# Optimization experiments

Measured on AMD Instinct MI355X. Metric: run time of the kernel, lower is better.

## Reference

```python
import jax, jax.numpy as jnp
import numpy as np

N = 50000      # nodes
E = 1600000    # edges (avg degree 32)
D_IN = 128
HID = 64


def setup_inputs() -> dict:
    key = jax.random.key(0)
    ks = jax.random.split(key, 7)
    x = jax.random.normal(ks[0], (N, D_IN), dtype=jnp.float32)
    ei = jax.random.randint(ks[1], (2, E), 0, N, dtype=jnp.int32)
    ew = jax.random.uniform(ks[2], (E,), dtype=jnp.float32)
    # GCNConv linear weights (glorot-ish scale); lin has no bias, conv bias added post-aggregation
    W1 = jax.random.normal(ks[3], (HID, D_IN), dtype=jnp.float32) * (1.0 / np.sqrt(D_IN))
    b1 = jnp.zeros((HID,), dtype=jnp.float32)
    W2 = jax.random.normal(ks[4], (HID, HID), dtype=jnp.float32) * (1.0 / np.sqrt(HID))
    b2 = jnp.zeros((HID,), dtype=jnp.float32)
    return {"x": x, "ei": ei, "ew": ew, "W1": W1, "b1": b1, "W2": W2, "b2": b2}


def _gcn_conv(x, src, dst, ew_all, W, b, n_nodes):
    """PyG GCNConv: gcn_norm (self-loops already appended) + x@W.T, gather-scale-scatter, +b."""
    deg = jax.ops.segment_sum(ew_all, dst, num_segments=n_nodes)  # dst-side weighted degree
    dinv = jnp.where(deg > 0, jax.lax.rsqrt(deg), 0.0)            # deg^{-1/2}, inf->0
    norm = dinv[src] * ew_all * dinv[dst]                          # [E+N]
    h = x @ W.T                                                    # [N, hid]
    msg = h[src] * norm[:, None]                                   # gather + scale
    out = jax.ops.segment_sum(msg, dst, num_segments=n_nodes)     # scatter-add
    return out + b


def reference(x, ei, ew, W1, b1, W2, b2):
    n_nodes = x.shape[0]
    # add self loops once (fill value 1.0), shared by both conv layers
    loop = jnp.arange(n_nodes, dtype=ei.dtype)
    src = jnp.concatenate([ei[0], loop])
    dst = jnp.concatenate([ei[1], loop])
    ew_all = jnp.concatenate([ew, jnp.ones((n_nodes,), dtype=ew.dtype)])

    h1 = jax.nn.relu(_gcn_conv(x, src, dst, ew_all, W1, b1, n_nodes))
    # dropout is identity in eval mode
    h2 = _gcn_conv(h1, src, dst, ew_all, W2, b2, n_nodes)
    return h2 + h1
```

## Files before the change

### kernel.cpp

```cpp
#include <hip/hip_runtime.h>

#define HID 64
#define DIN 128
#define NBLK 512

typedef unsigned long long ull;
typedef unsigned short u16;

static __device__ __forceinline__ u16 f2bf(float f) {
  unsigned u = __float_as_uint(f);
  unsigned lsb = (u >> 16) & 1u;
  u += 0x7fffu + lsb;
  return (u16)(u >> 16);
}


__global__ __launch_bounds__(512) void k_histA(const int* __restrict__ dst,
                                               int* __restrict__ G,
                                               int E, int NBC, int chunk,
                                               const float* __restrict__ W1,
                                               const float* __restrict__ W2,
                                               float* __restrict__ WT1,
                                               float* __restrict__ WT2) {
  int b = blockIdx.x, tid = threadIdx.x;
  if (b >= NBLK) {
    int idx = (b - NBLK) * 512 + tid;
    if (idx < DIN * 64) {
      int d = idx >> 6, j = idx & 63;
      WT1[idx] = W1[j * DIN + d];
    }
    int i2 = idx - DIN * 64;
    if (i2 >= 0 && i2 < HID * 64) {
      int d = i2 >> 6, j = i2 & 63;
      WT2[i2] = W2[j * HID + d];
    }
    return;
  }
  __shared__ int h[256];
  if (tid < 256) h[tid] = 0;
  __syncthreads();
  int e0 = b * chunk, e1 = min(E, e0 + chunk);
  for (int e = e0 + tid; e < e1; e += 512) atomicAdd(&h[dst[e] >> 8], 1);
  __syncthreads();
  if (tid < NBC) G[tid * NBLK + b] = h[tid];
}


__global__ __launch_bounds__(256) void k_chunksum(const int* __restrict__ G, int* bsum, int L) {
  int b = blockIdx.x, t = threadIdx.x;
  int base = b * 2048;
  int s = 0;
  for (int i = t; i < 2048; i += 256) {
    int g = base + i;
    s += (g < L) ? G[g] : 0;
  }
  __shared__ int red[4];
  for (int o = 32; o > 0; o >>= 1) s += __shfl_down(s, o);
  if ((t & 63) == 0) red[t >> 6] = s;
  __syncthreads();
  if (t == 0) bsum[b] = red[0] + red[1] + red[2] + red[3];
}

__global__ __launch_bounds__(64) void k_scanbsum(int* bsum, int nb) {
  int lane = threadIdx.x;
  int v = (lane < nb) ? bsum[lane] : 0;
  int incl = v;
  for (int o = 1; o < 64; o <<= 1) {
    int u = __shfl_up(incl, o);
    if (lane >= o) incl += u;
  }
  if (lane < nb) bsum[lane] = incl - v;
}

__global__ __launch_bounds__(256) void k_scanfinal(int* G, const int* __restrict__ bsum, int L) {
  int b = blockIdx.x, t = threadIdx.x;
  int i0 = b * 2048 + t * 8;
  int v[8], tsum = 0;
#pragma unroll
  for (int k = 0; k < 8; ++k) {
    v[k] = (i0 + k < L) ? G[i0 + k] : 0;
    tsum += v[k];
  }
  int incl = tsum;
  for (int o = 1; o < 64; o <<= 1) {
    int u = __shfl_up(incl, o);
    if ((t & 63) >= o) incl += u;
  }
  int wexcl = incl - tsum;
  __shared__ int wtot[4];
  int w = t >> 6;
  if ((t & 63) == 63) wtot[w] = incl;
  __syncthreads();
  int wbase = 0;
  for (int i = 0; i < w; ++i) wbase += wtot[i];
  int run = bsum[b] + wbase + wexcl;
#pragma unroll
  for (int k = 0; k < 8; ++k) {
    if (i0 + k < L) G[i0 + k] = run;
    run += v[k];
  }
}


__global__ __launch_bounds__(512) void k_scatterA(const int* __restrict__ src,
                                                  const int* __restrict__ dst,
                                                  const float* __restrict__ ew,
                                                  const int* __restrict__ Gs,
                                                  int2* __restrict__ bufA,
                                                  int E, int NBC, int chunk) {
  __shared__ int cur[256];
  int b = blockIdx.x, tid = threadIdx.x;
  if (tid < NBC) cur[tid] = Gs[tid * NBLK + b];
  __syncthreads();
  int e0 = b * chunk, e1 = min(E, e0 + chunk);
  for (int e = e0 + tid; e < e1; e += 512) {
    int s = src[e], d = dst[e];
    float w = ew[e];
    int p = atomicAdd(&cur[d >> 8], 1);
    bufA[p] = make_int2(__float_as_int(w), (int)(((unsigned)s << 16) | (unsigned)d));
  }
}


__global__ __launch_bounds__(512) void k_passB(const int2* __restrict__ bufA,
                                               const int* __restrict__ Gs,
                                               int2* __restrict__ bufB,
                                               int* __restrict__ offs,
                                               float* __restrict__ dinv,
                                               int NBC, int E, int N) {
  int bin = blockIdx.x, tid = threadIdx.x;
  __shared__ int h2[256];
  __shared__ int cur[256];
  __shared__ float dg[256];
  int base = Gs[bin * NBLK];
  int end  = (bin + 1 < NBC) ? Gs[(bin + 1) * NBLK] : E;
  int m = end - base;
  if (tid < 256) { h2[tid] = 0; dg[tid] = 0.f; }
  __syncthreads();
  for (int i = tid; i < m; i += 512) {
    unsigned sd = (unsigned)bufA[base + i].y;
    atomicAdd(&h2[sd & 255], 1);
  }
  __syncthreads();
  int own = (tid < 256) ? h2[tid] : 0;
  for (int o = 1; o < 256; o <<= 1) {
    int u = 0;
    if (tid < 256 && tid >= o) u = h2[tid - o];
    __syncthreads();
    if (tid < 256) h2[tid] += u;
    __syncthreads();
  }
  int nd = (bin << 8) + tid;
  if (tid < 256) {
    int excl = h2[tid] - own;
    cur[tid] = excl;
    if (nd < N) offs[nd] = base + excl;
  }
  if (bin == NBC - 1 && tid == 0) offs[N] = E;
  __syncthreads();
  for (int i = tid; i < m; i += 512) {
    int2 r = bufA[base + i];
    unsigned sd = (unsigned)r.y;
    int dl = (int)(sd & 255u);
    int p = atomicAdd(&cur[dl], 1);
    bufB[base + p] = r;
    atomicAdd(&dg[dl], __int_as_float(r.x));
  }
  __syncthreads();
  if (tid < 256 && nd < N) dinv[nd] = rsqrtf(1.0f + dg[tid]);
}


__global__ __launch_bounds__(256) void k_norm(int2* __restrict__ recs,
                                              const float* __restrict__ dinv, int E) {
  int e = blockIdx.x * 256 + threadIdx.x;
  if (e < E) {
    int2 r = recs[e];
    unsigned sd = (unsigned)r.y;
    int s = (int)(sd >> 16), d = (int)(sd & 0xffffu);
    float nrm = dinv[s] * __int_as_float(r.x) * dinv[d];
    recs[e] = make_int2(__float_as_int(nrm), s);
  }
}


template <int K>
__global__ __launch_bounds__(256) void k_gemm(const float* __restrict__ X,
                                              const float* __restrict__ WTg,
                                              u16* __restrict__ out, int n_nodes) {
  constexpr int PAD = 68;
  __shared__ float XT[64 * PAD];
  __shared__ float WL[64 * PAD];
  const int tid = threadIdx.x;
  const int n0 = blockIdx.x * 64;
  const int tx = tid & 15;
  const int ty = tid >> 4;
  float acc[4][4] = {{0.f}};

  for (int ph = 0; ph < K / 64; ++ph) {
    const int d0 = ph * 64;
    __syncthreads();
#pragma unroll
    for (int k = 0; k < 4; ++k) {
      int f = tid + k * 256;
      int r = f >> 4, q = f & 15;
      int n = n0 + r;
      float4 xv = (n < n_nodes)
        ? *reinterpret_cast<const float4*>(&X[(size_t)n * K + d0 + 4 * q])
        : make_float4(0.f, 0.f, 0.f, 0.f);
      *reinterpret_cast<float4*>(&XT[r * PAD + 4 * q]) = xv;
      float4 wv = *reinterpret_cast<const float4*>(&WTg[(size_t)(d0 + r) * 64 + 4 * q]);
      *reinterpret_cast<float4*>(&WL[r * PAD + 4 * q]) = wv;
    }
    __syncthreads();
#pragma unroll 4
    for (int dd = 0; dd < 64; dd += 4) {
      float4 xs[4], ws[4];
#pragma unroll
      for (int mi = 0; mi < 4; ++mi)
        xs[mi] = *reinterpret_cast<const float4*>(&XT[(4 * ty + mi) * PAD + dd]);
#pragma unroll
      for (int dk = 0; dk < 4; ++dk)
        ws[dk] = *reinterpret_cast<const float4*>(&WL[(dd + dk) * PAD + 4 * tx]);
#pragma unroll
      for (int mi = 0; mi < 4; ++mi) {
        float xm[4] = {xs[mi].x, xs[mi].y, xs[mi].z, xs[mi].w};
#pragma unroll
        for (int dk = 0; dk < 4; ++dk) {
          acc[mi][0] = fmaf(xm[dk], ws[dk].x, acc[mi][0]);
          acc[mi][1] = fmaf(xm[dk], ws[dk].y, acc[mi][1]);
          acc[mi][2] = fmaf(xm[dk], ws[dk].z, acc[mi][2]);
          acc[mi][3] = fmaf(xm[dk], ws[dk].w, acc[mi][3]);
        }
      }
    }
  }

#pragma unroll
  for (int mi = 0; mi < 4; ++mi) {
    int n = n0 + 4 * ty + mi;
    if (n < n_nodes) {
      ushort4 o = make_ushort4(f2bf(acc[mi][0]), f2bf(acc[mi][1]),
                               f2bf(acc[mi][2]), f2bf(acc[mi][3]));
      *reinterpret_cast<ushort4*>(&out[(size_t)n * HID + 4 * tx]) = o;
    }
  }
}


__device__ __forceinline__ void bfma8(const uint4& v, float w, float* a) {
  a[0] = fmaf(__uint_as_float(v.x << 16), w, a[0]);
  a[1] = fmaf(__uint_as_float(v.x & 0xffff0000u), w, a[1]);
  a[2] = fmaf(__uint_as_float(v.y << 16), w, a[2]);
  a[3] = fmaf(__uint_as_float(v.y & 0xffff0000u), w, a[3]);
  a[4] = fmaf(__uint_as_float(v.z << 16), w, a[4]);
  a[5] = fmaf(__uint_as_float(v.z & 0xffff0000u), w, a[5]);
  a[6] = fmaf(__uint_as_float(v.w << 16), w, a[6]);
  a[7] = fmaf(__uint_as_float(v.w & 0xffff0000u), w, a[7]);
}

__global__ __launch_bounds__(256) void k_agg(const u16* __restrict__ h,
                                             const int2* __restrict__ recs,
                                             const int* __restrict__ offs,
                                             const float* __restrict__ dinv,
                                             const float* __restrict__ bias,
                                             const float* __restrict__ resid,
                                             float* __restrict__ out, int n_nodes, int mode) {
  int tid = threadIdx.x;
  int lane = tid & 63;
  int g = lane >> 3;
  int p8 = (lane & 7) * 8;
  int node = (blockIdx.x * 4 + (tid >> 6)) * 8 + g;
  if (node >= n_nodes) return;
  int beg = offs[node], end = offs[node + 1];
  float di = dinv[node];

  float a[8], b[8];
  {
    uint4 v = *reinterpret_cast<const uint4*>(&h[(size_t)node * HID + p8]);
    float w = di * di;
    a[0] = __uint_as_float(v.x << 16) * w;
    a[1] = __uint_as_float(v.x & 0xffff0000u) * w;
    a[2] = __uint_as_float(v.y << 16) * w;
    a[3] = __uint_as_float(v.y & 0xffff0000u) * w;
    a[4] = __uint_as_float(v.z << 16) * w;
    a[5] = __uint_as_float(v.z & 0xffff0000u) * w;
    a[6] = __uint_as_float(v.w << 16) * w;
    a[7] = __uint_as_float(v.w & 0xffff0000u) * w;
#pragma unroll
    for (int j = 0; j < 8; ++j) b[j] = 0.f;
  }

  int i = beg;
  while (i + 8 <= end) {
    int2 r0 = recs[i];     int2 r1 = recs[i + 1];
    int2 r2 = recs[i + 2]; int2 r3 = recs[i + 3];
    int2 r4 = recs[i + 4]; int2 r5 = recs[i + 5];
    int2 r6 = recs[i + 6]; int2 r7 = recs[i + 7];
    uint4 v0 = *reinterpret_cast<const uint4*>(&h[(size_t)r0.y * HID + p8]);
    uint4 v1 = *reinterpret_cast<const uint4*>(&h[(size_t)r1.y * HID + p8]);
    uint4 v2 = *reinterpret_cast<const uint4*>(&h[(size_t)r2.y * HID + p8]);
    uint4 v3 = *reinterpret_cast<const uint4*>(&h[(size_t)r3.y * HID + p8]);
    uint4 v4 = *reinterpret_cast<const uint4*>(&h[(size_t)r4.y * HID + p8]);
    uint4 v5 = *reinterpret_cast<const uint4*>(&h[(size_t)r5.y * HID + p8]);
    uint4 v6 = *reinterpret_cast<const uint4*>(&h[(size_t)r6.y * HID + p8]);
    uint4 v7 = *reinterpret_cast<const uint4*>(&h[(size_t)r7.y * HID + p8]);
    bfma8(v0, __int_as_float(r0.x), a);
    bfma8(v1, __int_as_float(r1.x), b);
    bfma8(v2, __int_as_float(r2.x), a);
    bfma8(v3, __int_as_float(r3.x), b);
    bfma8(v4, __int_as_float(r4.x), a);
    bfma8(v5, __int_as_float(r5.x), b);
    bfma8(v6, __int_as_float(r6.x), a);
    bfma8(v7, __int_as_float(r7.x), b);
    i += 8;
  }
  if (i + 4 <= end) {
    int2 r0 = recs[i];     int2 r1 = recs[i + 1];
    int2 r2 = recs[i + 2]; int2 r3 = recs[i + 3];
    uint4 v0 = *reinterpret_cast<const uint4*>(&h[(size_t)r0.y * HID + p8]);
    uint4 v1 = *reinterpret_cast<const uint4*>(&h[(size_t)r1.y * HID + p8]);
    uint4 v2 = *reinterpret_cast<const uint4*>(&h[(size_t)r2.y * HID + p8]);
    uint4 v3 = *reinterpret_cast<const uint4*>(&h[(size_t)r3.y * HID + p8]);
    bfma8(v0, __int_as_float(r0.x), a);
    bfma8(v1, __int_as_float(r1.x), b);
    bfma8(v2, __int_as_float(r2.x), a);
    bfma8(v3, __int_as_float(r3.x), b);
    i += 4;
  }
  if (i + 2 <= end) {
    int2 r0 = recs[i];     int2 r1 = recs[i + 1];
    uint4 v0 = *reinterpret_cast<const uint4*>(&h[(size_t)r0.y * HID + p8]);
    uint4 v1 = *reinterpret_cast<const uint4*>(&h[(size_t)r1.y * HID + p8]);
    bfma8(v0, __int_as_float(r0.x), a);
    bfma8(v1, __int_as_float(r1.x), b);
    i += 2;
  }
  if (i < end) {
    int2 r0 = recs[i];
    uint4 v0 = *reinterpret_cast<const uint4*>(&h[(size_t)r0.y * HID + p8]);
    bfma8(v0, __int_as_float(r0.x), a);
  }

  float r[8];
#pragma unroll
  for (int j = 0; j < 8; ++j) r[j] = a[j] + b[j];
  float4 bb0 = *reinterpret_cast<const float4*>(&bias[p8]);
  float4 bb1 = *reinterpret_cast<const float4*>(&bias[p8 + 4]);
  r[0] += bb0.x; r[1] += bb0.y; r[2] += bb0.z; r[3] += bb0.w;
  r[4] += bb1.x; r[5] += bb1.y; r[6] += bb1.z; r[7] += bb1.w;
  if (mode == 0) {
#pragma unroll
    for (int j = 0; j < 8; ++j) r[j] = fmaxf(r[j], 0.f);
  } else {
    float4 rs0 = *reinterpret_cast<const float4*>(&resid[(size_t)node * HID + p8]);
    float4 rs1 = *reinterpret_cast<const float4*>(&resid[(size_t)node * HID + p8 + 4]);
    r[0] += rs0.x; r[1] += rs0.y; r[2] += rs0.z; r[3] += rs0.w;
    r[4] += rs1.x; r[5] += rs1.y; r[6] += rs1.z; r[7] += rs1.w;
  }
  *reinterpret_cast<float4*>(&out[(size_t)node * HID + p8]) =
      make_float4(r[0], r[1], r[2], r[3]);
  *reinterpret_cast<float4*>(&out[(size_t)node * HID + p8 + 4]) =
      make_float4(r[4], r[5], r[6], r[7]);
}


extern "C" void kernel_launch(void* const* d_in, const int* in_sizes, int n_in,
                              void* d_out, int out_size, void* d_ws, size_t ws_size,
                              hipStream_t stream) {
  const float* x  = (const float*)d_in[0];
  const int*   ei = (const int*)d_in[1];
  const float* ew = (const float*)d_in[2];
  const float* W1 = (const float*)d_in[3];
  const float* b1 = (const float*)d_in[4];
  const float* W2 = (const float*)d_in[5];
  const float* b2 = (const float*)d_in[6];
  float* out = (float*)d_out;

  const int N = in_sizes[0] / DIN;
  const int E = in_sizes[2];
  const int* src = ei;
  const int* dst = ei + E;

  const int NBC = (N + 255) >> 8;
  const int L = NBC * NBLK;
  const int chunk = (E + NBLK - 1) / NBLK;
  const int nch = (L + 2047) / 2048;

  char* p = (char*)d_ws;
  auto carve = [&](size_t bytes) {
    char* r = p;
    p += (bytes + 255) & ~(size_t)255;
    return r;
  };
  int*   G     = (int*)carve((size_t)L * 4);
  int*   bsum  = (int*)carve(64 * 4);
  int*   offs  = (int*)carve((size_t)(N + 1) * 4);
  float* dinv  = (float*)carve((size_t)N * 4);
  int2*  bufA  = (int2*)carve((size_t)E * 8);
  int2*  bufB  = (int2*)carve((size_t)E * 8);
  u16*   h     = (u16*)carve((size_t)N * HID * 2);
  float* h1    = (float*)carve((size_t)N * HID * 4);
  float* WT1   = (float*)carve((size_t)DIN * HID * 4);
  float* WT2   = (float*)carve((size_t)HID * HID * 4);

  int gblk = (N + 63) / 64;
  int ablk = (N + 31) / 32;
  int tblk = ((DIN + HID) * 64 + 511) / 512;

  k_histA<<<NBLK + tblk, 512, 0, stream>>>(dst, G, E, NBC, chunk, W1, W2, WT1, WT2);
  k_chunksum<<<nch, 256, 0, stream>>>(G, bsum, L);
  k_scanbsum<<<1, 64, 0, stream>>>(bsum, nch);
  k_scanfinal<<<nch, 256, 0, stream>>>(G, bsum, L);
  k_scatterA<<<NBLK, 512, 0, stream>>>(src, dst, ew, G, bufA, E, NBC, chunk);
  k_passB<<<NBC, 512, 0, stream>>>(bufA, G, bufB, offs, dinv, NBC, E, N);
  k_norm<<<(E + 255) / 256, 256, 0, stream>>>(bufB, dinv, E);

  k_gemm<DIN><<<gblk, 256, 0, stream>>>(x, WT1, h, N);
  k_agg<<<ablk, 256, 0, stream>>>(h, bufB, offs, dinv, b1, nullptr, h1, N, 0);
  k_gemm<HID><<<gblk, 256, 0, stream>>>(h1, WT2, h, N);
  k_agg<<<ablk, 256, 0, stream>>>(h, bufB, offs, dinv, b2, h1, out, N, 1);
}
```

Before: 229.2 us.

## Replace three-kernel scan with single-block bin scan and atomic cursors; fuse norm into gemm

Replaces the three-kernel exclusive scan over the per-block histogram with one single-block kernel that computes only per-bin totals and bases. Each scatter block now reserves its slice of a bin through an atomicAdd on a global cursor. The edge-normalisation pass is folded into the first GEMM launch as extra blocks, and NBLK is halved. This cuts kernel launches and scan traffic, at the cost of nondeterministic intra-bin ordering and fewer histogram blocks.

```diff
diff --git a/kernel.cpp b/kernel.cpp
--- a/kernel.cpp
+++ b/kernel.cpp
@@ -2,7 +2,7 @@
 
 #define HID 64
 #define DIN 128
-#define NBLK 512
+#define NBLK 256
 
 typedef unsigned long long ull;
 typedef unsigned short u16;
@@ -46,71 +46,52 @@
 }
 
 
-__global__ __launch_bounds__(256) void k_chunksum(const int* __restrict__ G, int* bsum, int L) {
-  int b = blockIdx.x, t = threadIdx.x;
-  int base = b * 2048;
-  int s = 0;
-  for (int i = t; i < 2048; i += 256) {
-    int g = base + i;
-    s += (g < L) ? G[g] : 0;
-  }
-  __shared__ int red[4];
-  for (int o = 32; o > 0; o >>= 1) s += __shfl_down(s, o);
-  if ((t & 63) == 0) red[t >> 6] = s;
-  __syncthreads();
-  if (t == 0) bsum[b] = red[0] + red[1] + red[2] + red[3];
-}
-
-__global__ __launch_bounds__(64) void k_scanbsum(int* bsum, int nb) {
-  int lane = threadIdx.x;
-  int v = (lane < nb) ? bsum[lane] : 0;
-  int incl = v;
-  for (int o = 1; o < 64; o <<= 1) {
-    int u = __shfl_up(incl, o);
-    if (lane >= o) incl += u;
-  }
-  if (lane < nb) bsum[lane] = incl - v;
-}
-
-__global__ __launch_bounds__(256) void k_scanfinal(int* G, const int* __restrict__ bsum, int L) {
-  int b = blockIdx.x, t = threadIdx.x;
-  int i0 = b * 2048 + t * 8;
-  int v[8], tsum = 0;
-#pragma unroll
-  for (int k = 0; k < 8; ++k) {
-    v[k] = (i0 + k < L) ? G[i0 + k] : 0;
-    tsum += v[k];
-  }
-  int incl = tsum;
-  for (int o = 1; o < 64; o <<= 1) {
-    int u = __shfl_up(incl, o);
-    if ((t & 63) >= o) incl += u;
-  }
-  int wexcl = incl - tsum;
-  __shared__ int wtot[4];
-  int w = t >> 6;
-  if ((t & 63) == 63) wtot[w] = incl;
-  __syncthreads();
-  int wbase = 0;
-  for (int i = 0; i < w; ++i) wbase += wtot[i];
-  int run = bsum[b] + wbase + wexcl;
-#pragma unroll
-  for (int k = 0; k < 8; ++k) {
-    if (i0 + k < L) G[i0 + k] = run;
-    run += v[k];
-  }
+__global__ __launch_bounds__(1024) void k_scan196(const int* __restrict__ G,
+                                                  int* __restrict__ base,
+                                                  int* __restrict__ cursor,
+                                                  int NBC, int E) {
+  __shared__ int tot[256];
+  int tid = threadIdx.x;
+  int w = tid >> 6, lane = tid & 63;
+  if (tid < 256) tot[tid] = 0;
+  __syncthreads();
+  for (int t = w; t < NBC; t += 16) {
+    int s = 0;
+    for (int b = lane; b < NBLK; b += 64) s += G[t * NBLK + b];
+    for (int o = 32; o > 0; o >>= 1) s += __shfl_down(s, o);
+    if (lane == 0) tot[t] = s;
+  }
+  __syncthreads();
+  int own = (tid < 256) ? tot[tid] : 0;
+  for (int o = 1; o < 256; o <<= 1) {
+    int u = 0;
+    if (tid < 256 && tid >= o) u = tot[tid - o];
+    __syncthreads();
+    if (tid < 256) tot[tid] += u;
+    __syncthreads();
+  }
+  if (tid < 256) {
+    int excl = tot[tid] - own;
+    base[tid] = excl;
+    cursor[tid] = excl;
+  }
+  if (tid == 0) base[256] = E;
 }
 
 
 __global__ __launch_bounds__(512) void k_scatterA(const int* __restrict__ src,
                                                   const int* __restrict__ dst,
                                                   const float* __restrict__ ew,
-                                                  const int* __restrict__ Gs,
+                                                  const int* __restrict__ G,
+                                                  int* __restrict__ cursor,
                                                   int2* __restrict__ bufA,
                                                   int E, int NBC, int chunk) {
   __shared__ int cur[256];
   int b = blockIdx.x, tid = threadIdx.x;
-  if (tid < NBC) cur[tid] = Gs[tid * NBLK + b];
+  if (tid < NBC) {
+    int myh = G[tid * NBLK + b];
+    cur[tid] = atomicAdd(&cursor[tid], myh);
+  }
   __syncthreads();
   int e0 = b * chunk, e1 = min(E, e0 + chunk);
   for (int e = e0 + tid; e < e1; e += 512) {
@@ -123,7 +104,7 @@
 
 
 __global__ __launch_bounds__(512) void k_passB(const int2* __restrict__ bufA,
-                                               const int* __restrict__ Gs,
+                                               const int* __restrict__ base,
                                                int2* __restrict__ bufB,
                                                int* __restrict__ offs,
                                                float* __restrict__ dinv,
@@ -132,13 +113,13 @@
   __shared__ int h2[256];
   __shared__ int cur[256];
   __shared__ float dg[256];
-  int base = Gs[bin * NBLK];
-  int end  = (bin + 1 < NBC) ? Gs[(bin + 1) * NBLK] : E;
-  int m = end - base;
+  int bbase = base[bin];
+  int bend  = base[bin + 1];
+  int m = bend - bbase;
   if (tid < 256) { h2[tid] = 0; dg[tid] = 0.f; }
   __syncthreads();
   for (int i = tid; i < m; i += 512) {
-    unsigned sd = (unsigned)bufA[base + i].y;
+    unsigned sd = (unsigned)bufA[bbase + i].y;
     atomicAdd(&h2[sd & 255], 1);
   }
   __syncthreads();
@@ -154,44 +135,45 @@
   if (tid < 256) {
     int excl = h2[tid] - own;
     cur[tid] = excl;
-    if (nd < N) offs[nd] = base + excl;
+    if (nd < N) offs[nd] = bbase + excl;
   }
   if (bin == NBC - 1 && tid == 0) offs[N] = E;
   __syncthreads();
   for (int i = tid; i < m; i += 512) {
-    int2 r = bufA[base + i];
+    int2 r = bufA[bbase + i];
     unsigned sd = (unsigned)r.y;
     int dl = (int)(sd & 255u);
     int p = atomicAdd(&cur[dl], 1);
-    bufB[base + p] = r;
+    bufB[bbase + p] = r;
     atomicAdd(&dg[dl], __int_as_float(r.x));
   }
   __syncthreads();
   if (tid < 256 && nd < N) dinv[nd] = rsqrtf(1.0f + dg[tid]);
-}
-
-
-__global__ __launch_bounds__(256) void k_norm(int2* __restrict__ recs,
-                                              const float* __restrict__ dinv, int E) {
-  int e = blockIdx.x * 256 + threadIdx.x;
-  if (e < E) {
-    int2 r = recs[e];
-    unsigned sd = (unsigned)r.y;
-    int s = (int)(sd >> 16), d = (int)(sd & 0xffffu);
-    float nrm = dinv[s] * __int_as_float(r.x) * dinv[d];
-    recs[e] = make_int2(__float_as_int(nrm), s);
-  }
 }
 
 
 template <int K>
 __global__ __launch_bounds__(256) void k_gemm(const float* __restrict__ X,
                                               const float* __restrict__ WTg,
-                                              u16* __restrict__ out, int n_nodes) {
+                                              u16* __restrict__ out, int n_nodes,
+                                              int2* __restrict__ recs,
+                                              const float* __restrict__ dinv,
+                                              int E, int gblk) {
+  const int tid = threadIdx.x;
+  if ((int)blockIdx.x >= gblk) {
+    int nb = gridDim.x - gblk;
+    for (int e = ((int)blockIdx.x - gblk) * 256 + tid; e < E; e += nb * 256) {
+      int2 r = recs[e];
+      unsigned sd = (unsigned)r.y;
+      int s = (int)(sd >> 16), d = (int)(sd & 0xffffu);
+      float nrm = dinv[s] * __int_as_float(r.x) * dinv[d];
+      recs[e] = make_int2(__float_as_int(nrm), s);
+    }
+    return;
+  }
   constexpr int PAD = 68;
   __shared__ float XT[64 * PAD];
   __shared__ float WL[64 * PAD];
-  const int tid = threadIdx.x;
   const int n0 = blockIdx.x * 64;
   const int tx = tid & 15;
   const int ty = tid >> 4;
@@ -383,9 +365,7 @@
   const int* dst = ei + E;
 
   const int NBC = (N + 255) >> 8;
-  const int L = NBC * NBLK;
   const int chunk = (E + NBLK - 1) / NBLK;
-  const int nch = (L + 2047) / 2048;
 
   char* p = (char*)d_ws;
   auto carve = [&](size_t bytes) {
@@ -393,31 +373,30 @@
     p += (bytes + 255) & ~(size_t)255;
     return r;
   };
-  int*   G     = (int*)carve((size_t)L * 4);
-  int*   bsum  = (int*)carve(64 * 4);
-  int*   offs  = (int*)carve((size_t)(N + 1) * 4);
-  float* dinv  = (float*)carve((size_t)N * 4);
-  int2*  bufA  = (int2*)carve((size_t)E * 8);
-  int2*  bufB  = (int2*)carve((size_t)E * 8);
-  u16*   h     = (u16*)carve((size_t)N * HID * 2);
-  float* h1    = (float*)carve((size_t)N * HID * 4);
-  float* WT1   = (float*)carve((size_t)DIN * HID * 4);
-  float* WT2   = (float*)carve((size_t)HID * HID * 4);
+  int*   G      = (int*)carve((size_t)256 * NBLK * 4);
+  int*   base   = (int*)carve(257 * 4);
+  int*   cursor = (int*)carve(256 * 4);
+  int*   offs   = (int*)carve((size_t)(N + 1) * 4);
+  float* dinv   = (float*)carve((size_t)N * 4);
+  int2*  bufA   = (int2*)carve((size_t)E * 8);
+  int2*  bufB   = (int2*)carve((size_t)E * 8);
+  u16*   h      = (u16*)carve((size_t)N * HID * 2);
+  float* h1     = (float*)carve((size_t)N * HID * 4);
+  float* WT1    = (float*)carve((size_t)DIN * HID * 4);
+  float* WT2    = (float*)carve((size_t)HID * HID * 4);
 
   int gblk = (N + 63) / 64;
   int ablk = (N + 31) / 32;
   int tblk = ((DIN + HID) * 64 + 511) / 512;
+  int nblk = (E + 1023) / 1024;
 
   k_histA<<<NBLK + tblk, 512, 0, stream>>>(dst, G, E, NBC, chunk, W1, W2, WT1, WT2);
-  k_chunksum<<<nch, 256, 0, stream>>>(G, bsum, L);
-  k_scanbsum<<<1, 64, 0, stream>>>(bsum, nch);
-  k_scanfinal<<<nch, 256, 0, stream>>>(G, bsum, L);
-  k_scatterA<<<NBLK, 512, 0, stream>>>(src, dst, ew, G, bufA, E, NBC, chunk);
-  k_passB<<<NBC, 512, 0, stream>>>(bufA, G, bufB, offs, dinv, NBC, E, N);
-  k_norm<<<(E + 255) / 256, 256, 0, stream>>>(bufB, dinv, E);
-
-  k_gemm<DIN><<<gblk, 256, 0, stream>>>(x, WT1, h, N);
+  k_scan196<<<1, 1024, 0, stream>>>(G, base, cursor, NBC, E);
+  k_scatterA<<<NBLK, 512, 0, stream>>>(src, dst, ew, G, cursor, bufA, E, NBC, chunk);
+  k_passB<<<NBC, 512, 0, stream>>>(bufA, base, bufB, offs, dinv, NBC, E, N);
+
+  k_gemm<DIN><<<gblk + nblk, 256, 0, stream>>>(x, WT1, h, N, bufB, dinv, E, gblk);
   k_agg<<<ablk, 256, 0, stream>>>(h, bufB, offs, dinv, b1, nullptr, h1, N, 0);
-  k_gemm<HID><<<gblk, 256, 0, stream>>>(h1, WT2, h, N);
+  k_gemm<HID><<<gblk, 256, 0, stream>>>(h1, WT2, h, N, nullptr, nullptr, 0, gblk);
   k_agg<<<ablk, 256, 0, stream>>>(h, bufB, offs, dinv, b2, h1, out, N, 1);
 }
```

After: 235.6 us. 1.03x slower.
